# Kernel optimization log

Measured on AMD Instinct MI355X. Metric: run time of the kernel, lower is better.

Reference implementation:

```python
import jax, jax.numpy as jnp
import numpy as np

NUM_HEADS = 16
NUM_UNITS = 1024
NEG = -2.0**32 + 1.0
EPS = 1e-8


def setup_inputs() -> dict:
    key = jax.random.key(0)
    ks = jax.random.split(key, 8)
    B, T, C = 2, 2048, 1024
    U = NUM_UNITS
    x = jax.random.normal(ks[0], (B, T, C), dtype=jnp.float32)
    s = 1.0 / np.sqrt(C)
    Wq = jax.random.normal(ks[1], (C, U), dtype=jnp.float32) * s
    Wk = jax.random.normal(ks[2], (C, U), dtype=jnp.float32) * s
    Wv = jax.random.normal(ks[3], (C, U), dtype=jnp.float32) * s
    bq = jnp.zeros((U,), dtype=jnp.float32)
    bk = jnp.zeros((U,), dtype=jnp.float32)
    bv = jnp.zeros((U,), dtype=jnp.float32)
    gamma = jnp.ones((U,), dtype=jnp.float32)
    beta = jnp.zeros((U,), dtype=jnp.float32)
    return {"x": x, "Wq": Wq, "bq": bq, "Wk": Wk, "bk": bk,
            "Wv": Wv, "bv": bv, "gamma": gamma, "beta": beta}


def _attention(x, Wq, bq, Wk, bk, Wv, bv, gamma, beta):
    B, T, C = x.shape
    H = NUM_HEADS
    U = NUM_UNITS
    dh = U // H
    # Dense projections with relu activation (Keras Dense(activation='relu'))
    Q = jax.nn.relu(x @ Wq + bq)  # [B, T, U]
    K = jax.nn.relu(x @ Wk + bk)
    V = jax.nn.relu(x @ Wv + bv)
    # split into heads: tf.split(axis=2) + concat(axis=0) == [B, T, H, dh]
    Qh = Q.reshape(B, T, H, dh)
    Kh = K.reshape(B, T, H, dh)
    Vh = V.reshape(B, T, H, dh)
    # scaled dot-product scores: scale by sqrt(d_head) (K_ last dim after split)
    scores = jnp.einsum('bqhd,bkhd->bhqk', Qh, Kh) / np.sqrt(dh)
    # key mask: sign(|sum(keys, -1)|) over the ORIGINAL keys input (= x)
    key_mask = jnp.sign(jnp.abs(jnp.sum(x, axis=-1)))  # [B, Tk]
    scores = jnp.where(key_mask[:, None, None, :] == 0, NEG, scores)
    # causal mask (lower-triangular)
    tril = jnp.tril(jnp.ones((T, T), dtype=scores.dtype))
    scores = jnp.where(tril[None, None, :, :] == 0, NEG, scores)
    attn = jax.nn.softmax(scores, axis=-1)
    # query mask: multiply attention rows for zero queries
    query_mask = jnp.sign(jnp.abs(jnp.sum(x, axis=-1)))  # [B, Tq]
    attn = attn * query_mask[:, None, :, None]
    # dropout rate is 0 -> identity
    out = jnp.einsum('bhqk,bkhd->bqhd', attn, Vh).reshape(B, T, U)
    # residual with original queries
    out = out + x
    # layer norm over last axis (tf.nn.moments: biased variance)
    mean = jnp.mean(out, axis=-1, keepdims=True)
    var = jnp.mean((out - mean) ** 2, axis=-1, keepdims=True)
    normalized = (out - mean) / jnp.sqrt(var + EPS)
    return gamma * normalized + beta


def reference(x, Wq, bq, Wk, bk, Wv, bv, gamma, beta):
    return _attention(x, Wq, bq, Wk, bk, Wv, bv, gamma, beta)
```

## Files before the change

### kernel.cpp

```cpp
#include <hip/hip_runtime.h>
#include <math.h>

#define BB 2
#define TT 2048
#define CC 1024
#define UU 1024
#define HH 16
#define DH 64
#define BT (BB*TT)

typedef __attribute__((ext_vector_type(8))) __bf16 bf16x8;
typedef __attribute__((ext_vector_type(4))) __bf16 bf16x4;
typedef __attribute__((ext_vector_type(4))) float f32x4;

#define GLL16(g, l) __builtin_amdgcn_global_load_lds( \
    (__attribute__((address_space(1))) const void*)(g), \
    (__attribute__((address_space(3))) void*)(l), 16, 0, 0)

#define C2EXP 0.18033688011112042f
#define MBIAS 64.0f

__global__ __launch_bounds__(256) void prep_kernel(
    const float* __restrict__ x, float* __restrict__ kadd, __bf16* __restrict__ xb,
    const float* __restrict__ Wq, const float* __restrict__ Wk,
    const float* __restrict__ Wv, __bf16* __restrict__ Wt) {
    const int bx = blockIdx.x;
    const int t = threadIdx.x;
    if (bx < BT) {
        int row = bx;
        float4 v = *(const float4*)&x[(size_t)row * CC + t * 4];
        bf16x4 o;
        o[0] = (__bf16)v.x; o[1] = (__bf16)v.y; o[2] = (__bf16)v.z; o[3] = (__bf16)v.w;
        *(bf16x4*)&xb[(size_t)row * CC + t * 4] = o;
        float s = v.x + v.y + v.z + v.w;
#pragma unroll
        for (int off = 32; off; off >>= 1) s += __shfl_down(s, off, 64);
        __shared__ float red[4];
        int lane = t & 63, w = t >> 6;
        if (lane == 0) red[w] = s;
        __syncthreads();
        if (t == 0) {
            float tot = red[0] + red[1] + red[2] + red[3];
            kadd[row] = (tot == 0.f ? -1.0e30f : 0.f) - MBIAS;
        }
    } else {
        int bz = bx - BT;
        int z = bz >> 8, rem = bz & 255;
        const float* W = z == 0 ? Wq : (z == 1 ? Wk : Wv);
        __bf16* Out = Wt + (size_t)z * CC * UU;
        __shared__ float tile[64][65];
        int n0 = (rem & 15) * 64, k0 = (rem >> 4) * 64;
        int r = t >> 4, c4 = (t & 15) * 4;
#pragma unroll
        for (int i = 0; i < 4; ++i) {
            float4 v = *(const float4*)&W[(size_t)(k0 + r + i * 16) * UU + n0 + c4];
            tile[r + i * 16][c4 + 0] = v.x; tile[r + i * 16][c4 + 1] = v.y;
            tile[r + i * 16][c4 + 2] = v.z; tile[r + i * 16][c4 + 3] = v.w;
        }
        __syncthreads();
#pragma unroll
        for (int i = 0; i < 4; ++i) {
            int nr = r + i * 16;
            bf16x4 o;
            o[0] = (__bf16)tile[c4 + 0][nr]; o[1] = (__bf16)tile[c4 + 1][nr];
            o[2] = (__bf16)tile[c4 + 2][nr]; o[3] = (__bf16)tile[c4 + 3][nr];
            *(bf16x4*)&Out[(size_t)(n0 + nr) * CC + k0 + c4] = o;
        }
    }
}

__global__ __launch_bounds__(256, 4) void qkv_mfma(
    const __bf16* __restrict__ xb, const __bf16* __restrict__ Wt_all,
    const float* __restrict__ bq, const float* __restrict__ bk,
    const float* __restrict__ bv,
    __bf16* __restrict__ Qo, __bf16* __restrict__ Ko, __bf16* __restrict__ VTo) {
    const int z = blockIdx.z;
    const __bf16* Wt = Wt_all + (size_t)z * CC * UU;
    const float* bias = z == 0 ? bq : (z == 1 ? bk : bv);

    const int m0 = blockIdx.x * 128, n0 = blockIdx.y * 128;
    const int t = threadIdx.x, w = t >> 6, lane = t & 63;
    const int quad = lane >> 4, nn = lane & 15;
    const int wr = w >> 1, wc = w & 1;

    __shared__ __bf16 smem[2 * 128 * 64];
    __bf16* As = smem;
    __bf16* Bs = smem + 128 * 64;

    f32x4 acc[4][4];
#pragma unroll
    for (int i = 0; i < 4; ++i)
#pragma unroll
        for (int j = 0; j < 4; ++j) acc[i][j] = (f32x4){0.f, 0.f, 0.f, 0.f};

    for (int k0 = 0; k0 < CC; k0 += 64) {
        __syncthreads();
#pragma unroll
        for (int i = 0; i < 4; ++i) {
            int c = i * 256 + t;
            int row = c >> 3;
            int gc = ((c & 7) ^ (row & 7)) * 8;
            GLL16(&xb[(size_t)(m0 + row) * CC + k0 + gc], &As[c * 8]);
            GLL16(&Wt[(size_t)(n0 + row) * CC + k0 + gc], &Bs[c * 8]);
        }
        __syncthreads();
#pragma unroll
        for (int kk = 0; kk < 2; ++kk) {
            bf16x8 af[4], bfr[4];
#pragma unroll
            for (int i = 0; i < 4; ++i) {
                int R = wr * 64 + i * 16 + nn;
                af[i] = *(const bf16x8*)&As[R * 64 + (((kk * 4 + quad) ^ (R & 7)) * 8)];
            }
#pragma unroll
            for (int j = 0; j < 4; ++j) {
                int R = wc * 64 + j * 16 + nn;
                bfr[j] = *(const bf16x8*)&Bs[R * 64 + (((kk * 4 + quad) ^ (R & 7)) * 8)];
            }
#pragma unroll
            for (int i = 0; i < 4; ++i)
#pragma unroll
                for (int j = 0; j < 4; ++j)
                    acc[i][j] = __builtin_amdgcn_mfma_f32_16x16x32_bf16(af[i], bfr[j], acc[i][j], 0, 0, 0);
        }
    }

    __bf16* cw = &smem[w * 1024];
    float bv4[4];
#pragma unroll
    for (int j = 0; j < 4; ++j) bv4[j] = bias[n0 + wc * 64 + j * 16 + nn];

    __syncthreads();

    if (z < 2) {
        __bf16* Out = z == 0 ? Qo : Ko;
#pragma unroll
        for (int i = 0; i < 4; ++i) {
#pragma unroll
            for (int j = 0; j < 4; ++j)
#pragma unroll
                for (int r = 0; r < 4; ++r)
                    cw[(quad * 4 + r) * 64 + j * 16 + nn] =
                        (__bf16)fmaxf(acc[i][j][r] + bv4[j], 0.f);
            int rr = lane >> 2, cc = (lane & 3) * 16;
            bf16x8 v0 = *(const bf16x8*)&cw[rr * 64 + cc];
            bf16x8 v1 = *(const bf16x8*)&cw[rr * 64 + cc + 8];
            size_t o = (size_t)(m0 + wr * 64 + i * 16 + rr) * UU + n0 + wc * 64 + cc;
            *(bf16x8*)&Out[o] = v0;
            *(bf16x8*)&Out[o + 8] = v1;
        }
    } else {
#pragma unroll
        for (int i = 0; i < 4; ++i) {
#pragma unroll
            for (int j = 0; j < 4; ++j)
#pragma unroll
                for (int r = 0; r < 4; ++r)
                    cw[(j * 16 + nn) * 16 + quad * 4 + r] =
                        (__bf16)fmaxf(acc[i][j][r] + bv4[j], 0.f);
            bf16x8 v0 = *(const bf16x8*)&cw[lane * 16];
            bf16x8 v1 = *(const bf16x8*)&cw[lane * 16 + 8];
            size_t o = (size_t)(n0 + wc * 64 + lane) * BT + m0 + wr * 64 + i * 16;
            *(bf16x8*)&VTo[o] = v0;
            *(bf16x8*)&VTo[o + 8] = v1;
        }
    }
}

__global__ __launch_bounds__(256, 4) void attn_mfma(
    const __bf16* __restrict__ Q, const __bf16* __restrict__ K,
    const __bf16* __restrict__ Vt, const float* __restrict__ kadd,
    __bf16* __restrict__ Obf, float* __restrict__ Op0, float* __restrict__ Op1,
    float* __restrict__ lq0, float* __restrict__ lq1) {
    const int bh = blockIdx.x, b = bh >> 4, h = bh & 15;
    const int cx = blockIdx.y;
    const int p = (cx & 7) | ((cx >> 4) << 3);
    const int half = (cx >> 3) & 1;
    const int col0 = h * 64, rowbase = b * TT;
    const int qa = p, qb = 31 - p;

    const int t = threadIdx.x;
    const int w = t >> 6, lane = t & 63, quad = lane >> 4, nn = lane & 15;
    const int s7 = nn & 7;

    __shared__ __align__(16) __bf16 ks[2][64 * 64];
    __shared__ __align__(16) __bf16 vt[2][64 * 64];
    __shared__ __align__(16) __bf16 ps[64 * 64];

    const int c0 = t;
    const int r0 = c0 >> 3, g0 = ((c0 & 7) ^ (r0 & 7)) * 8;
    const int prow = 16 * w + nn;

    const size_t KSTRIDE = 64 * (size_t)UU;
    const __bf16* kb0 = &K[(size_t)(rowbase + r0) * UU + col0 + g0];
    const __bf16* kb1 = kb0 + 32 * (size_t)UU;
    const __bf16* vb0 = &Vt[(size_t)(col0 + r0) * BT + rowbase + g0];
    const __bf16* vb1 = vb0 + 32 * (size_t)BT;
    const float* kab = &kadd[rowbase + quad * 4];

#define STAGE_TILE(BUF, KP0, KP1, VP0, VP1)   \
    GLL16((KP0), &ks[BUF][c0 * 8]);           \
    GLL16((KP1), &ks[BUF][c0 * 8 + 2048]);    \
    GLL16((VP0), &vt[BUF][c0 * 8]);           \
    GLL16((VP1), &vt[BUF][c0 * 8 + 2048]);

#define LOADKA(KT)                            \
    _Pragma("unroll")                         \
    for (int ct = 0; ct < 4; ++ct)            \
        ka[ct] = *(const f32x4*)&kab[(KT) * 64 + ct * 16];

    float lpA = 0.f, lpB = 0.f;
    f32x4 ocA[4], ocB[4];
#pragma unroll
    for (int dt = 0; dt < 4; ++dt) {
        ocA[dt] = (f32x4){0.f, 0.f, 0.f, 0.f};
        ocB[dt] = (f32x4){0.f, 0.f, 0.f, 0.f};
    }
    int cur = 0;
    f32x4 ka[4];
    bf16x8 bqA0, bqA1, bqB0, bqB1;

#define ATTN_CORE(KSC, VTC, DIAG, BQ0, BQ1, LP, OC)                            \
  {                                                                            \
    const __bf16* ksc = (KSC);                                                 \
    const __bf16* vtc = (VTC);                                                 \
    _Pragma("unroll")                                                          \
    for (int ct = 0; ct < 4; ++ct) {                                           \
      int krow = ct * 16 + nn;                                                 \
      bf16x8 a0 = *(const bf16x8*)&ksc[krow * 64 + ((quad ^ s7) * 8)];         \
      bf16x8 a1 = *(const bf16x8*)&ksc[krow * 64 + (((4 + quad) ^ s7) * 8)];   \
      f32x4 sc = (f32x4){0.f, 0.f, 0.f, 0.f};                                  \
      __builtin_amdgcn_s_setprio(1);                                           \
      sc = __builtin_amdgcn_mfma_f32_16x16x32_bf16(a0, (BQ0), sc, 0, 0, 0);    \
      sc = __builtin_amdgcn_mfma_f32_16x16x32_bf16(a1, (BQ1), sc, 0, 0, 0);    \
      __builtin_amdgcn_s_setprio(0);                                           \
      bf16x4 pw;                                                               \
      _Pragma("unroll")                                                        \
      for (int r = 0; r < 4; ++r) {                                            \
        float arg = fmaf(sc[r], C2EXP, ka[ct][r]);                             \
        if (DIAG) {                                                            \
          int kl = ct * 16 + quad * 4 + r;                                     \
          if (kl > prow) arg = -1.0e30f;                                       \
        }                                                                      \
        float pv = __builtin_amdgcn_exp2f(arg);                                \
        (LP) += pv;                                                            \
        pw[r] = (__bf16)pv;                                                    \
      }                                                                        \
      int chunk = ct * 2 + (quad >> 1);                                        \
      *(bf16x4*)&ps[prow * 64 + ((chunk ^ s7) * 8) + (quad & 1) * 4] = pw;     \
    }                                                                          \
    bf16x8 bp0 = *(const bf16x8*)&ps[prow * 64 + ((quad ^ s7) * 8)];           \
    bf16x8 bp1 = *(const bf16x8*)&ps[prow * 64 + (((4 + quad) ^ s7) * 8)];     \
    __builtin_amdgcn_s_setprio(1);                                             \
    _Pragma("unroll")                                                          \
    for (int dt = 0; dt < 4; ++dt) {                                           \
      int vrow = dt * 16 + nn;                                                 \
      bf16x8 a0 = *(const bf16x8*)&vtc[vrow * 64 + ((quad ^ s7) * 8)];         \
      bf16x8 a1 = *(const bf16x8*)&vtc[vrow * 64 + (((4 + quad) ^ s7) * 8)];   \
      (OC)[dt] = __builtin_amdgcn_mfma_f32_16x16x32_bf16(a0, bp0, (OC)[dt], 0, 0, 0); \
      (OC)[dt] = __builtin_amdgcn_mfma_f32_16x16x32_bf16(a1, bp1, (OC)[dt], 0, 0, 0); \
    }                                                                          \
    __builtin_amdgcn_s_setprio(0);                                             \
  }

    if (half == 0) {
        const int nA = qa + 1, nB = 16 - p;
        const int nmax = nA > nB ? nA : nB;
        {
            const __bf16* qrp = &Q[(size_t)(rowbase + qa * 64 + prow) * UU + col0];
            bqA0 = *(const bf16x8*)&qrp[quad * 8];
            bqA1 = *(const bf16x8*)&qrp[32 + quad * 8];
            const __bf16* qrq = &Q[(size_t)(rowbase + qb * 64 + prow) * UU + col0];
            bqB0 = *(const bf16x8*)&qrq[quad * 8];
            bqB1 = *(const bf16x8*)&qrq[32 + quad * 8];
        }
        const __bf16* kp0 = kb0; const __bf16* kp1 = kb1;
        const __bf16* vp0 = vb0; const __bf16* vp1 = vb1;
        STAGE_TILE(0, kp0, kp1, vp0, vp1)
        kp0 += KSTRIDE; kp1 += KSTRIDE; vp0 += 64; vp1 += 64;
        asm volatile("s_waitcnt vmcnt(0)" ::: "memory");
        __builtin_amdgcn_s_barrier();

        for (int kt = 0; kt < nmax; ++kt) {
            LOADKA(kt)
            __builtin_amdgcn_sched_barrier(0);
            if (kt + 1 < nmax) {
                STAGE_TILE(cur ^ 1, kp0, kp1, vp0, vp1)
                kp0 += KSTRIDE; kp1 += KSTRIDE; vp0 += 64; vp1 += 64;
            }
            __builtin_amdgcn_sched_barrier(0);
            if (kt < nA) {
                ATTN_CORE(ks[cur], vt[cur], kt == qa, bqA0, bqA1, lpA, ocA)
            }
            if (kt < nB) {
                ATTN_CORE(ks[cur], vt[cur], false, bqB0, bqB1, lpB, ocB)
            }
            cur ^= 1;
            if (kt + 1 < nmax) {
                asm volatile("s_waitcnt vmcnt(0)" ::: "memory");
                __builtin_amdgcn_s_barrier();
            }
        }
        {
            float l = lpA;
            l += __shfl_xor(l, 16, 64);
            l += __shfl_xor(l, 32, 64);
            const int grow = rowbase + qa * 64 + prow;
            float qsel = (kadd[grow] < -1.0e29f) ? 0.f : 1.f;
            float mult = qsel / fmaxf(l, 1e-37f);
#pragma unroll
            for (int dt = 0; dt < 4; ++dt) {
                bf16x4 ov;
                ov[0] = (__bf16)(ocA[dt][0] * mult); ov[1] = (__bf16)(ocA[dt][1] * mult);
                ov[2] = (__bf16)(ocA[dt][2] * mult); ov[3] = (__bf16)(ocA[dt][3] * mult);
                *(bf16x4*)&Obf[(size_t)grow * UU + col0 + dt * 16 + quad * 4] = ov;
            }
        }
        {
            float l = lpB;
            l += __shfl_xor(l, 16, 64);
            l += __shfl_xor(l, 32, 64);
            const int grow = rowbase + qb * 64 + prow;
            if (quad == 0) lq0[(size_t)grow * HH + h] = l;
            size_t orow = (size_t)(grow - (b + 1) * 1024);
#pragma unroll
            for (int dt = 0; dt < 4; ++dt)
                *(f32x4*)&Op0[orow * UU + col0 + dt * 16 + quad * 4] = ocB[dt];
        }
    } else {
        const int k0t = 16 - p;
        {
            const __bf16* qrow = &Q[(size_t)(rowbase + qb * 64 + prow) * UU + col0];
            bqA0 = *(const bf16x8*)&qrow[quad * 8];
            bqA1 = *(const bf16x8*)&qrow[32 + quad * 8];
        }
        const __bf16* kp0 = kb0 + (size_t)k0t * KSTRIDE;
        const __bf16* kp1 = kb1 + (size_t)k0t * KSTRIDE;
        const __bf16* vp0 = vb0 + k0t * 64;
        const __bf16* vp1 = vb1 + k0t * 64;
        STAGE_TILE(0, kp0, kp1, vp0, vp1)
        kp0 += KSTRIDE; kp1 += KSTRIDE; vp0 += 64; vp1 += 64;
        asm volatile("s_waitcnt vmcnt(0)" ::: "memory");
        __builtin_amdgcn_s_barrier();

        for (int i = 0; i < 15; ++i) {
            LOADKA(k0t + i)
            __builtin_amdgcn_sched_barrier(0);
            STAGE_TILE(cur ^ 1, kp0, kp1, vp0, vp1)
            kp0 += KSTRIDE; kp1 += KSTRIDE; vp0 += 64; vp1 += 64;
            __builtin_amdgcn_sched_barrier(0);
            ATTN_CORE(ks[cur], vt[cur], false, bqA0, bqA1, lpA, ocA)
            cur ^= 1;
            asm volatile("s_waitcnt vmcnt(0)" ::: "memory");
            __builtin_amdgcn_s_barrier();
        }
        LOADKA(k0t + 15)
        ATTN_CORE(ks[cur], vt[cur], true, bqA0, bqA1, lpA, ocA)
        {
            float l = lpA;
            l += __shfl_xor(l, 16, 64);
            l += __shfl_xor(l, 32, 64);
            const int grow = rowbase + qb * 64 + prow;
            if (quad == 0) lq1[(size_t)grow * HH + h] = l;
            size_t orow = (size_t)(grow - (b + 1) * 1024);
#pragma unroll
            for (int dt = 0; dt < 4; ++dt)
                *(f32x4*)&Op1[orow * UU + col0 + dt * 16 + quad * 4] = ocA[dt];
        }
    }
#undef ATTN_CORE
#undef STAGE_TILE
#undef LOADKA
}

__global__ __launch_bounds__(256) void ln_kernel(
    const __bf16* __restrict__ Obf, const float* __restrict__ Op0,
    const float* __restrict__ Op1, const float* __restrict__ lq0,
    const float* __restrict__ lq1, const float* __restrict__ kadd,
    const float* __restrict__ x, const float* __restrict__ gamma,
    const float* __restrict__ beta, float* __restrict__ out) {
    int row = blockIdx.x;
    int b = row >> 11;
    int qt = (row & (TT - 1)) >> 6;
    size_t base = (size_t)row * UU;
    int t = threadIdx.x;
    float v0, v1, v2, v3;
    float4 xv = *(const float4*)&x[base + t * 4];
    if (qt < 16) {
        bf16x4 ov = *(const bf16x4*)&Obf[base + t * 4];
        v0 = (float)ov[0] + xv.x; v1 = (float)ov[1] + xv.y;
        v2 = (float)ov[2] + xv.z; v3 = (float)ov[3] + xv.w;
    } else {
        int h = t >> 4;
        float l = lq0[(size_t)row * HH + h] + lq1[(size_t)row * HH + h];
        size_t base1 = (size_t)(row - (b + 1) * 1024) * UU;
        f32x4 o0 = *(const f32x4*)&Op0[base1 + t * 4];
        f32x4 o1 = *(const f32x4*)&Op1[base1 + t * 4];
        float qsel = (kadd[row] < -1.0e29f) ? 0.f : 1.f;
        float mult = qsel / fmaxf(l, 1e-37f);
        v0 = (o0[0] + o1[0]) * mult + xv.x; v1 = (o0[1] + o1[1]) * mult + xv.y;
        v2 = (o0[2] + o1[2]) * mult + xv.z; v3 = (o0[3] + o1[3]) * mult + xv.w;
    }
    float s1 = v0 + v1 + v2 + v3;
    float s2 = v0 * v0 + v1 * v1 + v2 * v2 + v3 * v3;
#pragma unroll
    for (int off = 32; off; off >>= 1) {
        s1 += __shfl_down(s1, off, 64);
        s2 += __shfl_down(s2, off, 64);
    }
    __shared__ float r1[4], r2[4];
    int lane = t & 63, w = t >> 6;
    if (lane == 0) { r1[w] = s1; r2[w] = s2; }
    __syncthreads();
    s1 = r1[0] + r1[1] + r1[2] + r1[3];
    s2 = r2[0] + r2[1] + r2[2] + r2[3];
    float mean = s1 * (1.0f / 1024.0f);
    float var = s2 * (1.0f / 1024.0f) - mean * mean;
    float rstd = rsqrtf(var + 1e-8f);
    float4 g = *(const float4*)&gamma[t * 4];
    float4 be = *(const float4*)&beta[t * 4];
    float4 ores;
    ores.x = g.x * (v0 - mean) * rstd + be.x;
    ores.y = g.y * (v1 - mean) * rstd + be.y;
    ores.z = g.z * (v2 - mean) * rstd + be.z;
    ores.w = g.w * (v3 - mean) * rstd + be.w;
    *(float4*)&out[base + t * 4] = ores;
}

extern "C" void kernel_launch(void* const* d_in, const int* in_sizes, int n_in,
                              void* d_out, int out_size, void* d_ws, size_t ws_size,
                              hipStream_t stream) {
    const float* x     = (const float*)d_in[0];
    const float* Wq    = (const float*)d_in[1];
    const float* bq    = (const float*)d_in[2];
    const float* Wk    = (const float*)d_in[3];
    const float* bk    = (const float*)d_in[4];
    const float* Wv    = (const float*)d_in[5];
    const float* bv    = (const float*)d_in[6];
    const float* gamma = (const float*)d_in[7];
    const float* beta  = (const float*)d_in[8];
    float* out = (float*)d_out;

    char* wsb = (char*)d_ws;
    const size_t MB = 1024ull * 1024;
    __bf16* xb  = (__bf16*)(wsb);
    __bf16* Wt  = (__bf16*)(wsb + 8 * MB);
    __bf16* Obf = (__bf16*)(wsb);
    float* Op0  = (float*)(wsb + 8 * MB);
    __bf16* Qb  = (__bf16*)(wsb + 16 * MB);
    __bf16* Kb  = (__bf16*)(wsb + 24 * MB);
    __bf16* Vt  = (__bf16*)(wsb + 32 * MB);
    float* kadd = (float*)(wsb + 40 * MB);
    float* Op1  = (float*)(wsb + 41 * MB);
    float* lq0  = (float*)(wsb + 49 * MB);
    float* lq1  = (float*)(wsb + 50 * MB);

    prep_kernel<<<dim3(BT + 768), dim3(256), 0, stream>>>(x, kadd, xb, Wq, Wk, Wv, Wt);
    qkv_mfma<<<dim3(BT / 128, UU / 128, 3), dim3(256), 0, stream>>>(
        xb, Wt, bq, bk, bv, Qb, Kb, Vt);
    attn_mfma<<<dim3(BB * HH, 32), dim3(256), 0, stream>>>(
        Qb, Kb, Vt, kadd, Obf, Op0, Op1, lq0, lq1);
    ln_kernel<<<dim3(BT), dim3(256), 0, stream>>>(
        Obf, Op0, Op1, lq0, lq1, kadd, x, gamma, beta, out);
}
```

Measured before the change: 163.3 us.

## Drop LDS staging of K/V tiles and read them directly from global memory

Removes the double-buffered LDS staging of K and V tiles (global_load_lds plus barriers) in the attention kernel. Each wave now loads its K rows and V^T rows straight from global memory into registers before the MFMAs. This removes LDS traffic, the per-tile barriers and the LDS footprint, which may raise occupancy. The cost is that each of the four waves fetches the same K/V data from global/L2, with no software prefetch to overlap the load latency.

Result: slower. 255.0 us (+56.1%).

```diff
diff --git a/kernel.cpp b/kernel.cpp
--- a/kernel.cpp
+++ b/kernel.cpp
@@ -168,7 +168,7 @@
 }
 
 __global__ __launch_bounds__(256, 4) void attn_mfma(
-    const __bf16* __restrict__ Q, const __bf16* __restrict__ K,
+    const __bf16* __restrict__ Kg, const __bf16* __restrict__ Q,
     const __bf16* __restrict__ Vt, const float* __restrict__ kadd,
     __bf16* __restrict__ Obf, float* __restrict__ Op0, float* __restrict__ Op1,
     float* __restrict__ lq0, float* __restrict__ lq1) {
@@ -183,26 +183,10 @@
     const int w = t >> 6, lane = t & 63, quad = lane >> 4, nn = lane & 15;
     const int s7 = nn & 7;
 
-    __shared__ __align__(16) __bf16 ks[2][64 * 64];
-    __shared__ __align__(16) __bf16 vt[2][64 * 64];
     __shared__ __align__(16) __bf16 ps[64 * 64];
 
-    const int c0 = t;
-    const int r0 = c0 >> 3, g0 = ((c0 & 7) ^ (r0 & 7)) * 8;
     const int prow = 16 * w + nn;
-
-    const size_t KSTRIDE = 64 * (size_t)UU;
-    const __bf16* kb0 = &K[(size_t)(rowbase + r0) * UU + col0 + g0];
-    const __bf16* kb1 = kb0 + 32 * (size_t)UU;
-    const __bf16* vb0 = &Vt[(size_t)(col0 + r0) * BT + rowbase + g0];
-    const __bf16* vb1 = vb0 + 32 * (size_t)BT;
     const float* kab = &kadd[rowbase + quad * 4];
-
-#define STAGE_TILE(BUF, KP0, KP1, VP0, VP1)   \
-    GLL16((KP0), &ks[BUF][c0 * 8]);           \
-    GLL16((KP1), &ks[BUF][c0 * 8 + 2048]);    \
-    GLL16((VP0), &vt[BUF][c0 * 8]);           \
-    GLL16((VP1), &vt[BUF][c0 * 8 + 2048]);
 
 #define LOADKA(KT)                            \
     _Pragma("unroll")                         \
@@ -216,19 +200,18 @@
         ocA[dt] = (f32x4){0.f, 0.f, 0.f, 0.f};
         ocB[dt] = (f32x4){0.f, 0.f, 0.f, 0.f};
     }
-    int cur = 0;
     f32x4 ka[4];
     bf16x8 bqA0, bqA1, bqB0, bqB1;
 
-#define ATTN_CORE(KSC, VTC, DIAG, BQ0, BQ1, LP, OC)                            \
+#define ATTN_CORE(KT, DIAG, BQ0, BQ1, LP, OC)                                  \
   {                                                                            \
-    const __bf16* ksc = (KSC);                                                 \
-    const __bf16* vtc = (VTC);                                                 \
+    const int k0g = (KT) * 64;                                                 \
     _Pragma("unroll")                                                          \
     for (int ct = 0; ct < 4; ++ct) {                                           \
       int krow = ct * 16 + nn;                                                 \
-      bf16x8 a0 = *(const bf16x8*)&ksc[krow * 64 + ((quad ^ s7) * 8)];         \
-      bf16x8 a1 = *(const bf16x8*)&ksc[krow * 64 + (((4 + quad) ^ s7) * 8)];   \
+      const __bf16* kr = &Kg[(size_t)(rowbase + k0g + krow) * UU + col0];      \
+      bf16x8 a0 = *(const bf16x8*)&kr[quad * 8];                               \
+      bf16x8 a1 = *(const bf16x8*)&kr[32 + quad * 8];                          \
       f32x4 sc = (f32x4){0.f, 0.f, 0.f, 0.f};                                  \
       __builtin_amdgcn_s_setprio(1);                                           \
       sc = __builtin_amdgcn_mfma_f32_16x16x32_bf16(a0, (BQ0), sc, 0, 0, 0);    \
@@ -255,8 +238,9 @@
     _Pragma("unroll")                                                          \
     for (int dt = 0; dt < 4; ++dt) {                                           \
       int vrow = dt * 16 + nn;                                                 \
-      bf16x8 a0 = *(const bf16x8*)&vtc[vrow * 64 + ((quad ^ s7) * 8)];         \
-      bf16x8 a1 = *(const bf16x8*)&vtc[vrow * 64 + (((4 + quad) ^ s7) * 8)];   \
+      const __bf16* vr = &Vt[(size_t)(col0 + vrow) * BT + rowbase + k0g];      \
+      bf16x8 a0 = *(const bf16x8*)&vr[quad * 8];                               \
+      bf16x8 a1 = *(const bf16x8*)&vr[32 + quad * 8];                          \
       (OC)[dt] = __builtin_amdgcn_mfma_f32_16x16x32_bf16(a0, bp0, (OC)[dt], 0, 0, 0); \
       (OC)[dt] = __builtin_amdgcn_mfma_f32_16x16x32_bf16(a1, bp1, (OC)[dt], 0, 0, 0); \
     }                                                                          \
@@ -274,31 +258,13 @@
             bqB0 = *(const bf16x8*)&qrq[quad * 8];
             bqB1 = *(const bf16x8*)&qrq[32 + quad * 8];
         }
-        const __bf16* kp0 = kb0; const __bf16* kp1 = kb1;
-        const __bf16* vp0 = vb0; const __bf16* vp1 = vb1;
-        STAGE_TILE(0, kp0, kp1, vp0, vp1)
-        kp0 += KSTRIDE; kp1 += KSTRIDE; vp0 += 64; vp1 += 64;
-        asm volatile("s_waitcnt vmcnt(0)" ::: "memory");
-        __builtin_amdgcn_s_barrier();
-
         for (int kt = 0; kt < nmax; ++kt) {
             LOADKA(kt)
-            __builtin_amdgcn_sched_barrier(0);
-            if (kt + 1 < nmax) {
-                STAGE_TILE(cur ^ 1, kp0, kp1, vp0, vp1)
-                kp0 += KSTRIDE; kp1 += KSTRIDE; vp0 += 64; vp1 += 64;
-            }
-            __builtin_amdgcn_sched_barrier(0);
             if (kt < nA) {
-                ATTN_CORE(ks[cur], vt[cur], kt == qa, bqA0, bqA1, lpA, ocA)
+                ATTN_CORE(kt, kt == qa, bqA0, bqA1, lpA, ocA)
             }
             if (kt < nB) {
-                ATTN_CORE(ks[cur], vt[cur], false, bqB0, bqB1, lpB, ocB)
-            }
-            cur ^= 1;
-            if (kt + 1 < nmax) {
-                asm volatile("s_waitcnt vmcnt(0)" ::: "memory");
-                __builtin_amdgcn_s_barrier();
+                ATTN_CORE(kt, false, bqB0, bqB1, lpB, ocB)
             }
         }
         {
@@ -334,28 +300,15 @@
             bqA0 = *(const bf16x8*)&qrow[quad * 8];
             bqA1 = *(const bf16x8*)&qrow[32 + quad * 8];
         }
-        const __bf16* kp0 = kb0 + (size_t)k0t * KSTRIDE;
-        const __bf16* kp1 = kb1 + (size_t)k0t * KSTRIDE;
-        const __bf16* vp0 = vb0 + k0t * 64;
-        const __bf16* vp1 = vb1 + k0t * 64;
-        STAGE_TILE(0, kp0, kp1, vp0, vp1)
-        kp0 += KSTRIDE; kp1 += KSTRIDE; vp0 += 64; vp1 += 64;
-        asm volatile("s_waitcnt vmcnt(0)" ::: "memory");
-        __builtin_amdgcn_s_barrier();
-
-        for (int i = 0; i < 15; ++i) {
-            LOADKA(k0t + i)
-            __builtin_amdgcn_sched_barrier(0);
-            STAGE_TILE(cur ^ 1, kp0, kp1, vp0, vp1)
-            kp0 += KSTRIDE; kp1 += KSTRIDE; vp0 += 64; vp1 += 64;
-            __builtin_amdgcn_sched_barrier(0);
-            ATTN_CORE(ks[cur], vt[cur], false, bqA0, bqA1, lpA, ocA)
-            cur ^= 1;
-            asm volatile("s_waitcnt vmcnt(0)" ::: "memory");
-            __builtin_amdgcn_s_barrier();
-        }
-        LOADKA(k0t + 15)
-        ATTN_CORE(ks[cur], vt[cur], true, bqA0, bqA1, lpA, ocA)
+        for (int i = 0; i < 16; ++i) {
+            const int kt = k0t + i;
+            LOADKA(kt)
+            if (i < 15) {
+                ATTN_CORE(kt, false, bqA0, bqA1, lpA, ocA)
+            } else {
+                ATTN_CORE(kt, true, bqA0, bqA1, lpA, ocA)
+            }
+        }
         {
             float l = lpA;
             l += __shfl_xor(l, 16, 64);
@@ -369,7 +322,6 @@
         }
     }
 #undef ATTN_CORE
-#undef STAGE_TILE
 #undef LOADKA
 }
 
@@ -459,7 +411,7 @@
     qkv_mfma<<<dim3(BT / 128, UU / 128, 3), dim3(256), 0, stream>>>(
         xb, Wt, bq, bk, bv, Qb, Kb, Vt);
     attn_mfma<<<dim3(BB * HH, 32), dim3(256), 0, stream>>>(
-        Qb, Kb, Vt, kadd, Obf, Op0, Op1, lq0, lq1);
+        Kb, Qb, Vt, kadd, Obf, Op0, Op1, lq0, lq1);
     ln_kernel<<<dim3(BT), dim3(256), 0, stream>>>(
         Obf, Op0, Op1, lq0, lq1, kadd, x, gamma, beta, out);
 }
```

## Enlarge QKV GEMM tiles to 256x256 with double-buffered async LDS pipeline

Applied to the files above, without the earlier changes.

Rewrites the QKV projection GEMM to use 256x256 block tiles with 512 threads (8 waves, each computing 128x64). The main loop now double-buffers LDS, interleaving global_load_lds prefetch of the next K-slice with MFMA work on the current one, using explicit vmcnt waits, sched barriers and s_setprio. The aim is to hide global-load latency and raise operand reuse per LDS byte. In exchange the grid drops to 192 blocks, fewer than the CU count, and each block uses 128KB of LDS, so occupancy and load balance may suffer.

New measurement: 166.8 us. 1.02x slower.

```diff
diff --git a/kernel.cpp b/kernel.cpp
--- a/kernel.cpp
+++ b/kernel.cpp
@@ -69,7 +69,7 @@
     }
 }
 
-__global__ __launch_bounds__(256, 4) void qkv_mfma(
+__global__ __launch_bounds__(512, 1) void qkv_mfma(
     const __bf16* __restrict__ xb, const __bf16* __restrict__ Wt_all,
     const float* __restrict__ bq, const float* __restrict__ bk,
     const float* __restrict__ bv,
@@ -78,64 +78,113 @@
     const __bf16* Wt = Wt_all + (size_t)z * CC * UU;
     const float* bias = z == 0 ? bq : (z == 1 ? bk : bv);
 
-    const int m0 = blockIdx.x * 128, n0 = blockIdx.y * 128;
+    const int m0 = blockIdx.x * 256, n0 = blockIdx.y * 256;
     const int t = threadIdx.x, w = t >> 6, lane = t & 63;
     const int quad = lane >> 4, nn = lane & 15;
-    const int wr = w >> 1, wc = w & 1;
-
-    __shared__ __bf16 smem[2 * 128 * 64];
-    __bf16* As = smem;
-    __bf16* Bs = smem + 128 * 64;
-
-    f32x4 acc[4][4];
-#pragma unroll
-    for (int i = 0; i < 4; ++i)
+    const int wm = w >> 2, wn = w & 3;
+
+    __shared__ __bf16 smem[4 * 256 * 64];
+
+    f32x4 acc[8][4];
+#pragma unroll
+    for (int i = 0; i < 8; ++i)
 #pragma unroll
         for (int j = 0; j < 4; ++j) acc[i][j] = (f32x4){0.f, 0.f, 0.f, 0.f};
 
-    for (int k0 = 0; k0 < CC; k0 += 64) {
-        __syncthreads();
-#pragma unroll
-        for (int i = 0; i < 4; ++i) {
-            int c = i * 256 + t;
-            int row = c >> 3;
-            int gc = ((c & 7) ^ (row & 7)) * 8;
-            GLL16(&xb[(size_t)(m0 + row) * CC + k0 + gc], &As[c * 8]);
-            GLL16(&Wt[(size_t)(n0 + row) * CC + k0 + gc], &Bs[c * 8]);
-        }
-        __syncthreads();
-#pragma unroll
-        for (int kk = 0; kk < 2; ++kk) {
-            bf16x8 af[4], bfr[4];
-#pragma unroll
-            for (int i = 0; i < 4; ++i) {
-                int R = wr * 64 + i * 16 + nn;
-                af[i] = *(const bf16x8*)&As[R * 64 + (((kk * 4 + quad) ^ (R & 7)) * 8)];
-            }
-#pragma unroll
-            for (int j = 0; j < 4; ++j) {
-                int R = wc * 64 + j * 16 + nn;
-                bfr[j] = *(const bf16x8*)&Bs[R * 64 + (((kk * 4 + quad) ^ (R & 7)) * 8)];
-            }
-#pragma unroll
-            for (int i = 0; i < 4; ++i)
-#pragma unroll
-                for (int j = 0; j < 4; ++j)
-                    acc[i][j] = __builtin_amdgcn_mfma_f32_16x16x32_bf16(af[i], bfr[j], acc[i][j], 0, 0, 0);
-        }
+    bf16x8 af[4][2], bfr[2][2];
+
+#define STAGE_A(I, DA, K0) { int c = (I) * 512 + t; int row = c >> 3;          \
+    int gc = ((c & 7) ^ (row & 7)) * 8;                                        \
+    GLL16(&xb[(size_t)(m0 + row) * CC + (K0) + gc], (DA) + c * 8); }
+#define STAGE_B(I, DB, K0) { int c = (I) * 512 + t; int row = c >> 3;          \
+    int gc = ((c & 7) ^ (row & 7)) * 8;                                        \
+    GLL16(&Wt[(size_t)(n0 + row) * CC + (K0) + gc], (DB) + c * 8); }
+#define LOAD_AF(IH, AS) _Pragma("unroll")                                      \
+    for (int ii = 0; ii < 4; ++ii) {                                           \
+        int R = wm * 128 + ((IH) * 4 + ii) * 16 + nn;                          \
+        af[ii][0] = *(const bf16x8*)&(AS)[R * 64 + ((quad ^ (R & 7)) * 8)];    \
+        af[ii][1] = *(const bf16x8*)&(AS)[R * 64 + (((4 + quad) ^ (R & 7)) * 8)]; }
+#define LOAD_BF(JH, BS) _Pragma("unroll")                                      \
+    for (int jj = 0; jj < 2; ++jj) {                                           \
+        int R = wn * 64 + ((JH) * 2 + jj) * 16 + nn;                           \
+        bfr[jj][0] = *(const bf16x8*)&(BS)[R * 64 + ((quad ^ (R & 7)) * 8)];   \
+        bfr[jj][1] = *(const bf16x8*)&(BS)[R * 64 + (((4 + quad) ^ (R & 7)) * 8)]; }
+#define MFMA16(IH, JH) __builtin_amdgcn_s_setprio(1);                          \
+    _Pragma("unroll")                                                          \
+    for (int ii = 0; ii < 4; ++ii)                                             \
+        _Pragma("unroll")                                                      \
+        for (int jj = 0; jj < 2; ++jj) {                                       \
+            acc[(IH)*4+ii][(JH)*2+jj] = __builtin_amdgcn_mfma_f32_16x16x32_bf16( \
+                af[ii][0], bfr[jj][0], acc[(IH)*4+ii][(JH)*2+jj], 0, 0, 0);    \
+            acc[(IH)*4+ii][(JH)*2+jj] = __builtin_amdgcn_mfma_f32_16x16x32_bf16( \
+                af[ii][1], bfr[jj][1], acc[(IH)*4+ii][(JH)*2+jj], 0, 0, 0); }  \
+    __builtin_amdgcn_s_setprio(0);
+
+    {
+        __bf16* A0 = smem;
+        __bf16* B0 = smem + 32768;
+        STAGE_B(0, B0, 0) STAGE_B(1, B0, 0) STAGE_B(2, B0, 0) STAGE_B(3, B0, 0)
+        STAGE_A(0, A0, 0) STAGE_A(1, A0, 0) STAGE_A(2, A0, 0) STAGE_A(3, A0, 0)
+    }
+
+    for (int ks = 0; ks < 15; ++ks) {
+        const int b = ks & 1;
+        __bf16* Ac = smem + b * 16384;
+        __bf16* Bc = smem + 32768 + b * 16384;
+        __bf16* An = smem + (b ^ 1) * 16384;
+        __bf16* Bn = smem + 32768 + (b ^ 1) * 16384;
+        const int k0n = (ks + 1) * 64;
+        STAGE_B(0, Bn, k0n) STAGE_B(1, Bn, k0n)
+        __builtin_amdgcn_sched_barrier(0);
+        asm volatile("s_waitcnt vmcnt(3)" ::: "memory");
+        __builtin_amdgcn_s_barrier();
+        LOAD_AF(0, Ac)
+        LOAD_BF(0, Bc)
+        MFMA16(0, 0)
+        __builtin_amdgcn_sched_barrier(0);
+        STAGE_B(2, Bn, k0n) STAGE_B(3, Bn, k0n)
+        LOAD_BF(1, Bc)
+        MFMA16(0, 1)
+        __builtin_amdgcn_sched_barrier(0);
+        STAGE_A(0, An, k0n) STAGE_A(1, An, k0n)
+        __builtin_amdgcn_sched_barrier(0);
+        asm volatile("s_waitcnt vmcnt(6)" ::: "memory");
+        __builtin_amdgcn_s_barrier();
+        LOAD_AF(1, Ac)
+        LOAD_BF(0, Bc)
+        MFMA16(1, 0)
+        __builtin_amdgcn_sched_barrier(0);
+        STAGE_A(2, An, k0n) STAGE_A(3, An, k0n)
+        LOAD_BF(1, Bc)
+        MFMA16(1, 1)
+        __builtin_amdgcn_s_barrier();
+    }
+    asm volatile("s_waitcnt vmcnt(0)" ::: "memory");
+    __builtin_amdgcn_s_barrier();
+    {
+        __bf16* Ac = smem + 16384;
+        __bf16* Bc = smem + 32768 + 16384;
+        LOAD_AF(0, Ac)
+        LOAD_BF(0, Bc)
+        MFMA16(0, 0)
+        LOAD_BF(1, Bc)
+        MFMA16(0, 1)
+        LOAD_AF(1, Ac)
+        LOAD_BF(0, Bc)
+        MFMA16(1, 0)
+        LOAD_BF(1, Bc)
+        MFMA16(1, 1)
     }
 
     __bf16* cw = &smem[w * 1024];
     float bv4[4];
 #pragma unroll
-    for (int j = 0; j < 4; ++j) bv4[j] = bias[n0 + wc * 64 + j * 16 + nn];
-
-    __syncthreads();
+    for (int j = 0; j < 4; ++j) bv4[j] = bias[n0 + wn * 64 + j * 16 + nn];
 
     if (z < 2) {
         __bf16* Out = z == 0 ? Qo : Ko;
 #pragma unroll
-        for (int i = 0; i < 4; ++i) {
+        for (int i = 0; i < 8; ++i) {
 #pragma unroll
             for (int j = 0; j < 4; ++j)
 #pragma unroll
@@ -145,13 +194,13 @@
             int rr = lane >> 2, cc = (lane & 3) * 16;
             bf16x8 v0 = *(const bf16x8*)&cw[rr * 64 + cc];
             bf16x8 v1 = *(const bf16x8*)&cw[rr * 64 + cc + 8];
-            size_t o = (size_t)(m0 + wr * 64 + i * 16 + rr) * UU + n0 + wc * 64 + cc;
+            size_t o = (size_t)(m0 + wm * 128 + i * 16 + rr) * UU + n0 + wn * 64 + cc;
             *(bf16x8*)&Out[o] = v0;
             *(bf16x8*)&Out[o + 8] = v1;
         }
     } else {
 #pragma unroll
-        for (int i = 0; i < 4; ++i) {
+        for (int i = 0; i < 8; ++i) {
 #pragma unroll
             for (int j = 0; j < 4; ++j)
 #pragma unroll
@@ -160,11 +209,16 @@
                         (__bf16)fmaxf(acc[i][j][r] + bv4[j], 0.f);
             bf16x8 v0 = *(const bf16x8*)&cw[lane * 16];
             bf16x8 v1 = *(const bf16x8*)&cw[lane * 16 + 8];
-            size_t o = (size_t)(n0 + wc * 64 + lane) * BT + m0 + wr * 64 + i * 16;
+            size_t o = (size_t)(n0 + wn * 64 + lane) * BT + m0 + wm * 128 + i * 16;
             *(bf16x8*)&VTo[o] = v0;
             *(bf16x8*)&VTo[o + 8] = v1;
         }
     }
+#undef MFMA16
+#undef LOAD_BF
+#undef LOAD_AF
+#undef STAGE_B
+#undef STAGE_A
 }
 
 __global__ __launch_bounds__(256, 4) void attn_mfma(
@@ -456,7 +510,7 @@
     float* lq1  = (float*)(wsb + 50 * MB);
 
     prep_kernel<<<dim3(BT + 768), dim3(256), 0, stream>>>(x, kadd, xb, Wq, Wk, Wv, Wt);
-    qkv_mfma<<<dim3(BT / 128, UU / 128, 3), dim3(256), 0, stream>>>(
+    qkv_mfma<<<dim3(BT / 256, UU / 256, 3), dim3(512), 0, stream>>>(
         xb, Wt, bq, bk, bv, Qb, Kb, Vt);
     attn_mfma<<<dim3(BB * HH, 32), dim3(256), 0, stream>>>(
         Qb, Kb, Vt, kadd, Obf, Op0, Op1, lq0, lq1);
```
